# Performance work log

Measured on AMD Instinct MI355X. Metric: run time of the kernel, lower is better.

## Reference

```python
import jax, jax.numpy as jnp
import numpy as np

AC_KERNEL = 5


def deconv(x, w, stride):
    """torch ConvTranspose2d(k=3, p=1, bias=False), stride 1 or 2 (output_padding=1).
    w has torch layout [Cin, Cout, kH, kW]."""
    wk = jnp.transpose(w, (1, 0, 2, 3))[:, :, ::-1, ::-1]  # OIHW, spatially flipped
    dn = ('NCHW', 'OIHW', 'NCHW')
    if stride == 1:
        return jax.lax.conv_general_dilated(x, wk, (1, 1), ((1, 1), (1, 1)), dimension_numbers=dn)
    # stride 2: dilate input, pad (k-1-p, k-1-p+op) = (1, 2) -> doubles H, W
    return jax.lax.conv_general_dilated(x, wk, (1, 1), ((1, 2), (1, 2)),
                                        lhs_dilation=(2, 2), dimension_numbers=dn)


def sepconv(feat, kv, kh, K):
    """Per-pixel adaptive separable convolution (Niklaus SepConv).
    feat: [B,C,H,W]; kv, kh: [B,K,H,W]. Replication-pad by K//2, then
    out[b,c,y,x] = sum_{i,j} pad[b,c,y+i,x+j] * kv[b,i,y,x] * kh[b,j,y,x]."""
    pad = K // 2
    B, C, H, W = feat.shape
    p = jnp.pad(feat, ((0, 0), (0, 0), (pad, pad), (pad, pad)), mode='edge')
    out = jnp.zeros_like(feat)
    for i in range(K):  # small fixed loop over kernel taps
        row = p[:, :, i:i + H, :]  # [B,C,H,W+2*pad]
        horiz = row[:, :, :, 0:W] * kh[:, 0:1]
        for j in range(1, K):
            horiz = horiz + row[:, :, :, j:j + W] * kh[:, j:j + 1]
        out = out + kv[:, i:i + 1] * horiz
    return out


def fusion(feat, kv, kh, mask):
    tmp = sepconv(feat, kv, kh, AC_KERNEL)
    return mask * tmp + (1.0 - mask) * feat


def setup_inputs() -> dict:
    key = jax.random.key(0)
    ks = jax.random.split(key, 20)
    B, G = 128, 64
    d = {'cont_feat': jax.random.normal(ks[0], (B, G, 8, 8), jnp.float32)}
    sizes = [8, 16, 32, 64]
    for li, s in enumerate(sizes):
        d[f'kv{li}'] = jax.random.uniform(ks[1 + 3 * li], (B, AC_KERNEL, s, s), jnp.float32)
        d[f'kh{li}'] = jax.random.uniform(ks[2 + 3 * li], (B, AC_KERNEL, s, s), jnp.float32)
        d[f'm{li}'] = jax.random.uniform(ks[3 + 3 * li], (B, 1, s, s), jnp.float32)
    wshapes = [(G, G * 8, 3, 3), (G * 8, G * 4, 3, 3), (G * 4, G * 2, 3, 3),
               (G * 2, G * 2, 3, 3), (G * 2, G, 3, 3), (G, 3, 3, 3)]
    for wi, ws in enumerate(wshapes):
        d[f'w{wi + 1}'] = jax.random.normal(ks[13 + wi], ws, jnp.float32) * 0.05
    return d


def reference(cont_feat, kv0, kh0, m0, kv1, kh1, m1, kv2, kh2, m2, kv3, kh3, m3,
              w1, w2, w3, w4, w5, w6):
    # kernel_layer = 4, no_mask = False, use_bn = False
    feat_8 = fusion(cont_feat, kv0, kh0, m0)                      # [B,G,8,8]
    feat_16 = jax.nn.relu(deconv(feat_8, w1, 2))                  # [B,8G,16,16]
    feat_16 = fusion(feat_16, kv1, kh1, m1)
    h = jax.nn.relu(deconv(feat_16, w2, 1))                       # [B,4G,16,16]
    feat_32 = jax.nn.relu(deconv(h, w3, 2))                       # [B,2G,32,32]
    feat_32 = fusion(feat_32, kv2, kh2, m2)
    h = jax.nn.relu(deconv(feat_32, w4, 1))                       # [B,2G,32,32]
    h = jax.nn.relu(deconv(h, w5, 2))                             # [B,G,64,64]
    out = jnp.tanh(deconv(h, w6, 1))                              # [B,3,64,64]
    out = fusion(out, kv3, kh3, m3)
    return (out, feat_8, feat_16, feat_32)
```

## Files before the change

### kernel.cpp

```cpp
#include <hip/hip_runtime.h>
#include <math.h>

typedef short v8s __attribute__((ext_vector_type(8)));
typedef float v16f __attribute__((ext_vector_type(16)));

__device__ inline unsigned short f2bf(float f) {
    union { float f; unsigned u; } c; c.f = f;
    unsigned r = (c.u + 0x7fffu + ((c.u >> 16) & 1u)) >> 16;
    return (unsigned short)r;
}

template<int LW>
__global__ __launch_bounds__(256) void fusion2_kernel(
        const float* __restrict__ feat, const float* __restrict__ kv,
        const float* __restrict__ kh, const float* __restrict__ m,
        float* __restrict__ out, int C, int CH, int H, int lhw) {
    constexpr int W = 1 << LW;
    const int t = blockIdx.x * 256 + threadIdx.x;
    const int hw = H << LW;
    const int b = t >> lhw;
    const int pix = t & (hw - 1);
    const int x = pix & (W - 1);
    const int y = pix >> LW;
    const int lane = threadIdx.x & 63;
    const int rowbase = (lane & ~(W - 1)) << 2;

    const int c0 = blockIdx.y * CH;

    const float mv = m[(size_t)b * hw + pix];
    float kvv[5], khv[5];
#pragma unroll
    for (int i = 0; i < 5; i++) {
        kvv[i] = kv[((size_t)b * 5 + i) * hw + pix];
        khv[i] = kh[((size_t)b * 5 + i) * hw + pix];
    }
    int idx[5];
#pragma unroll
    for (int j = 0; j < 5; j++) {
        int xx = x + j - 2; xx = xx < 0 ? 0 : (xx >= W ? W - 1 : xx);
        idx[j] = rowbase + (xx << 2);
    }
    int roff[5];
#pragma unroll
    for (int i = 0; i < 5; i++) {
        int yy = y + i - 2; yy = yy < 0 ? 0 : (yy >= H ? H - 1 : yy);
        roff[i] = (yy << LW) + x;
    }

    const float* fbase = feat + ((size_t)b * C + c0) * hw;
    float* obase = out + ((size_t)b * C + c0) * hw + pix;
    const float om = 1.f - mv;

#pragma unroll 4
    for (int cc = 0; cc < CH; cc++) {
        const float* q = fbase + (size_t)cc * hw;
        float s = 0.f;
        float fv = 0.f;
#pragma unroll
        for (int i = 0; i < 5; i++) {
            float v = q[roff[i]];
            if (i == 2) fv = v;
            int vb = __float_as_int(v);
            float h = 0.f;
#pragma unroll
            for (int j = 0; j < 5; j++) {
                float nv = __int_as_float(
                    __builtin_amdgcn_ds_bpermute(idx[j], vb));
                h += nv * khv[j];
            }
            s += kvv[i] * h;
        }
        obase[(size_t)cc * hw] = mv * s + om * fv;
    }
}

__global__ __launch_bounds__(256) void nchw_to_nhwc_bf16(
        const float* __restrict__ in, unsigned short* __restrict__ out,
        int C, int H, int W, int lw, int lc2) {
    extern __shared__ unsigned short sm_t[];
    const int y = blockIdx.x, b = blockIdx.y;
    const int Cp = C + 8;
    const int tid = threadIdx.x;
    for (int i = tid; i < C * W; i += 256) {
        int x = i & (W - 1), c = i >> lw;
        float v = in[(((size_t)b * C + c) * H + y) * W + x];
        sm_t[x * Cp + c] = f2bf(v);
    }
    __syncthreads();
    const unsigned* s32 = (const unsigned*)sm_t;
    unsigned* o32 = (unsigned*)(out + (((size_t)b * H + y) * W) * C);
    const int n32 = (W * C) >> 1;
    for (int i = tid; i < n32; i += 256) {
        int x = i >> lc2;
        int c2 = i - (x << lc2);
        o32[i] = s32[x * (Cp >> 1) + c2];
    }
}

__global__ __launch_bounds__(256) void repack_w_frag(
        const float* __restrict__ w, unsigned short* __restrict__ wk,
        int Cin, int Cout, int flip) {
    int idx = blockIdx.x * 256 + threadIdx.x;
    if (idx >= Cin * Cout) return;
    int ci = idx / Cout, co = idx - ci * Cout;
    const float* src = w + (size_t)idx * 9;
    const int nCb = Cout >> 5, nH = Cin >> 4;
    const size_t inner = (size_t)((((ci >> 3) & 1) * 32 + (co & 31)) * 8 + (ci & 7));
#pragma unroll
    for (int k = 0; k < 9; k++) {
        int t = flip ? (8 - k) : k;
        size_t blk = ((size_t)t * nCb + (co >> 5)) * nH + (ci >> 4);
        wk[(blk << 9) + inner] = f2bf(src[k]);
    }
}

template<int W, int TH, int LW>
__global__ __launch_bounds__(256) void conv3x3_mfma(
        const unsigned short* __restrict__ X,
        const unsigned short* __restrict__ Wk,
        unsigned short* __restrict__ out, int Cin, int Cout, int H) {
    constexpr int TP = (TH + 2) * (W + 2);
    __shared__ unsigned short sB[TP * 40];
    const int tid = threadIdx.x;
    const int lane = tid & 63, wv = tid >> 6;
    const int wm = wv >> 1, wn = wv & 1;
    const int y0 = blockIdx.x * TH;
    const int coB = blockIdx.y * 128 + wm * 64;
    const int b = blockIdx.z;
    const int n = lane & 31, kg = lane >> 5;
    const int p0 = wn * 64 + n, p1 = p0 + 32;
    const int r0 = p0 >> LW, c0 = p0 & (W - 1);
    const int r1 = p1 >> LW, c1 = p1 & (W - 1);
    const int bo0 = (r0 * (W + 2) + c0) * 40 + kg * 8;
    const int bo1 = (r1 * (W + 2) + c1) * 40 + kg * 8;
    v16f acc00 = {}, acc01 = {}, acc10 = {}, acc11 = {};
    const size_t cbStride = (size_t)(Cin >> 4) << 9;
    const size_t tStride  = (size_t)(Cout >> 5) * cbStride;
    const unsigned short* Af = Wk + (size_t)(coB >> 5) * cbStride + (lane << 3);
    const unsigned short* Xb = X + (size_t)b * H * W * Cin;

    for (int ci0 = 0; ci0 < Cin; ci0 += 32) {
        for (int i = tid; i < TP * 4; i += 256) {
            int pix = i >> 2, part = i & 3;
            int py = pix / (W + 2), px = pix - py * (W + 2);
            int gy = y0 + py - 1, gx = px - 1;
            uint4 v = make_uint4(0u, 0u, 0u, 0u);
            if (gy >= 0 && gy < H && (unsigned)gx < (unsigned)W)
                v = *(const uint4*)(Xb + ((size_t)(gy * W + gx)) * Cin + ci0 + part * 8);
            *(uint4*)(sB + pix * 40 + part * 8) = v;
        }
        __syncthreads();
#pragma unroll
        for (int t = 0; t < 9; t++) {
            const int ky = t / 3, kx = t - ky * 3;
            const int toff = (ky * (W + 2) + kx) * 40;
#pragma unroll
            for (int kh = 0; kh < 2; kh++) {
                const unsigned short* ap =
                    Af + (size_t)t * tStride + (size_t)(((ci0 >> 4) + kh) << 9);
                v8s A0 = *(const v8s*)(ap);
                v8s A1 = *(const v8s*)(ap + cbStride);
                v8s B0 = *(const v8s*)(sB + bo0 + toff + kh * 16);
                v8s B1 = *(const v8s*)(sB + bo1 + toff + kh * 16);
                acc00 = __builtin_amdgcn_mfma_f32_32x32x16_bf16(A0, B0, acc00, 0, 0, 0);
                acc01 = __builtin_amdgcn_mfma_f32_32x32x16_bf16(A0, B1, acc01, 0, 0, 0);
                acc10 = __builtin_amdgcn_mfma_f32_32x32x16_bf16(A1, B0, acc10, 0, 0, 0);
                acc11 = __builtin_amdgcn_mfma_f32_32x32x16_bf16(A1, B1, acc11, 0, 0, 0);
            }
        }
        __syncthreads();
    }
    unsigned short* ob = out + (size_t)b * H * W * Cout;
#pragma unroll
    for (int sm = 0; sm < 2; sm++) {
        v16f a0 = sm ? acc10 : acc00;
        v16f a1 = sm ? acc11 : acc01;
        const int cobase = coB + sm * 32 + 4 * kg;
        unsigned short* q0p = ob + ((size_t)((y0 + r0) * W + c0)) * Cout + cobase;
        unsigned short* q1p = ob + ((size_t)((y0 + r1) * W + c1)) * Cout + cobase;
#pragma unroll
        for (int r2 = 0; r2 < 4; r2++) {
            ushort4 q0, q1; float v;
            v = a0[4 * r2 + 0]; v = v > 0.f ? v : 0.f; q0.x = f2bf(v);
            v = a0[4 * r2 + 1]; v = v > 0.f ? v : 0.f; q0.y = f2bf(v);
            v = a0[4 * r2 + 2]; v = v > 0.f ? v : 0.f; q0.z = f2bf(v);
            v = a0[4 * r2 + 3]; v = v > 0.f ? v : 0.f; q0.w = f2bf(v);
            *(ushort4*)(q0p + 8 * r2) = q0;
            v = a1[4 * r2 + 0]; v = v > 0.f ? v : 0.f; q1.x = f2bf(v);
            v = a1[4 * r2 + 1]; v = v > 0.f ? v : 0.f; q1.y = f2bf(v);
            v = a1[4 * r2 + 2]; v = v > 0.f ? v : 0.f; q1.z = f2bf(v);
            v = a1[4 * r2 + 3]; v = v > 0.f ? v : 0.f; q1.w = f2bf(v);
            *(ushort4*)(q1p + 8 * r2) = q1;
        }
    }
}

template<int W, int TH, int NWN, int NWM, int LW>
__global__ __launch_bounds__(256) void deconv2_mfma(
        const unsigned short* __restrict__ X,
        const unsigned short* __restrict__ Wk,
        float* __restrict__ out, int Cin, int Cout, int Hin) {
    constexpr int ROWS = NWN * TH + 1;
    constexpr int NPIX = ROWS * (W + 1);
    __shared__ unsigned short sB[NPIX * 40];
    const int tid = threadIdx.x;
    const int lane = tid & 63, wv = tid >> 6;
    const int wm = wv / NWN, wn = wv % NWN;
    const int n = lane & 31, kg = lane >> 5;
    const int y0 = blockIdx.x * (NWN * TH);
    const int coB = (blockIdx.y * NWM + wm) * 64;
    const int b = blockIdx.z;
    const int Yl = wn * TH + (n >> LW);
    const int Xl = n & (W - 1);
    v16f zero = {};
    v16f acc[2][2][2];
#pragma unroll
    for (int i = 0; i < 2; i++)
#pragma unroll
        for (int j = 0; j < 2; j++)
#pragma unroll
            for (int s = 0; s < 2; s++) acc[i][j][s] = zero;
    const unsigned short* Xb = X + (size_t)b * Hin * W * Cin;
    const size_t cbStride = (size_t)(Cin >> 4) << 9;
    const size_t tStride  = (size_t)(Cout >> 5) * cbStride;
    const unsigned short* Af = Wk + (size_t)(coB >> 5) * cbStride + (lane << 3);
    const int PY[3] = {1, 0, 1}, DY[3] = {1, 0, 0};

    for (int ci0 = 0; ci0 < Cin; ci0 += 32) {
        for (int i = tid; i < NPIX * 4; i += 256) {
            int pix = i >> 2, part = i & 3;
            int py_ = pix / (W + 1), px_ = pix - py_ * (W + 1);
            int gy = y0 + py_, gx = px_;
            uint4 v = make_uint4(0u, 0u, 0u, 0u);
            if (gy < Hin && gx < W)
                v = *(const uint4*)(Xb + ((size_t)(gy * W + gx)) * Cin + ci0 + part * 8);
            *(uint4*)(sB + pix * 40 + part * 8) = v;
        }
        __syncthreads();
#pragma unroll
        for (int ky = 0; ky < 3; ky++) {
#pragma unroll
            for (int kx = 0; kx < 3; kx++) {
                const int py = PY[ky], dy = DY[ky];
                const int px = PY[kx], dx = DY[kx];
                const int t = ky * 3 + kx;
                const int boff = ((Yl + dy) * (W + 1) + (Xl + dx)) * 40 + kg * 8;
#pragma unroll
                for (int kh = 0; kh < 2; kh++) {
                    const unsigned short* ap =
                        Af + (size_t)t * tStride + (size_t)(((ci0 >> 4) + kh) << 9);
                    v8s B  = *(const v8s*)(sB + boff + kh * 16);
                    v8s A0 = *(const v8s*)(ap);
                    v8s A1 = *(const v8s*)(ap + cbStride);
                    acc[py][px][0] = __builtin_amdgcn_mfma_f32_32x32x16_bf16(A0, B, acc[py][px][0], 0, 0, 0);
                    acc[py][px][1] = __builtin_amdgcn_mfma_f32_32x32x16_bf16(A1, B, acc[py][px][1], 0, 0, 0);
                }
            }
        }
        __syncthreads();
    }
    const int Wo = 2 * W, Ho = 2 * Hin;
    const int yin = y0 + Yl;
#pragma unroll
    for (int py = 0; py < 2; py++) {
        const int oy = 2 * yin + py;
#pragma unroll
        for (int sm = 0; sm < 2; sm++) {
            const int cobase = coB + sm * 32 + 4 * kg;
#pragma unroll
            for (int r = 0; r < 16; r++) {
                int co = cobase + (r & 3) + 8 * (r >> 2);
                float v0 = acc[py][0][sm][r]; v0 = v0 > 0.f ? v0 : 0.f;
                float v1 = acc[py][1][sm][r]; v1 = v1 > 0.f ? v1 : 0.f;
                *(float2*)(out + (((size_t)(b * Cout + co) * Ho + oy) * Wo + 2 * Xl)) =
                    make_float2(v0, v1);
            }
        }
    }
}

__global__ __launch_bounds__(256) void conv_s1_c3_tanh_kernel(
        const float* __restrict__ in, const float* __restrict__ w,
        float* __restrict__ out, int Cin, int H, int W) {
    __shared__ float sIn[8][18][19];
    __shared__ float sW[8][3][9];
    const int tid = threadIdx.x;
    const int r = tid >> 4, c = tid & 15;
    const int ntx = W >> 4;
    const int tx0 = (blockIdx.x % ntx) << 4, ty0 = (blockIdx.x / ntx) << 4;
    const int b = blockIdx.z;
    const int hw = H * W;
    float acc[3] = {0.f, 0.f, 0.f};
    for (int ci0 = 0; ci0 < Cin; ci0 += 8) {
        for (int i = tid; i < 8 * 18 * 18; i += 256) {
            int ci = i / 324, rr = i % 324, ly = rr / 18, lx = rr % 18;
            int gy = ty0 + ly - 1, gx = tx0 + lx - 1;
            float v = 0.f;
            if (gy >= 0 && gy < H && gx >= 0 && gx < W)
                v = in[(size_t)(b * Cin + ci0 + ci) * hw + gy * W + gx];
            sIn[ci][ly][lx] = v;
        }
        for (int i = tid; i < 8 * 3 * 9; i += 256) {
            int ci = i / 27, rr = i % 27, co = rr / 9, k = rr % 9;
            sW[ci][co][k] = w[(size_t)((ci0 + ci) * 3 + co) * 9 + (8 - k)];
        }
        __syncthreads();
#pragma unroll
        for (int ci = 0; ci < 8; ci++) {
            float v00 = sIn[ci][r][c],     v01 = sIn[ci][r][c + 1],     v02 = sIn[ci][r][c + 2];
            float v10 = sIn[ci][r + 1][c], v11 = sIn[ci][r + 1][c + 1], v12 = sIn[ci][r + 1][c + 2];
            float v20 = sIn[ci][r + 2][c], v21 = sIn[ci][r + 2][c + 1], v22 = sIn[ci][r + 2][c + 2];
#pragma unroll
            for (int co = 0; co < 3; co++) {
                const float* wp = &sW[ci][co][0];
                acc[co] += v00 * wp[0] + v01 * wp[1] + v02 * wp[2]
                         + v10 * wp[3] + v11 * wp[4] + v12 * wp[5]
                         + v20 * wp[6] + v21 * wp[7] + v22 * wp[8];
            }
        }
        __syncthreads();
    }
#pragma unroll
    for (int co = 0; co < 3; co++)
        out[(size_t)(b * 3 + co) * hw + (ty0 + r) * W + tx0 + c] = tanhf(acc[co]);
}

extern "C" void kernel_launch(void* const* d_in, const int* in_sizes, int n_in,
                              void* d_out, int out_size, void* d_ws, size_t ws_size,
                              hipStream_t stream) {
    const float* cont = (const float*)d_in[0];
    const float* kv0 = (const float*)d_in[1];
    const float* kh0 = (const float*)d_in[2];
    const float* m0  = (const float*)d_in[3];
    const float* kv1 = (const float*)d_in[4];
    const float* kh1 = (const float*)d_in[5];
    const float* m1  = (const float*)d_in[6];
    const float* kv2 = (const float*)d_in[7];
    const float* kh2 = (const float*)d_in[8];
    const float* m2  = (const float*)d_in[9];
    const float* kv3 = (const float*)d_in[10];
    const float* kh3 = (const float*)d_in[11];
    const float* m3  = (const float*)d_in[12];
    const float* w1  = (const float*)d_in[13];
    const float* w2  = (const float*)d_in[14];
    const float* w3  = (const float*)d_in[15];
    const float* w4  = (const float*)d_in[16];
    const float* w5  = (const float*)d_in[17];
    const float* w6  = (const float*)d_in[18];

    float* out = (float*)d_out;
    float* f8  = out + 1572864;
    float* f16 = out + 2097152;
    float* f32 = out + 18874368;

    char* ws = (char*)d_ws;

    float* A0 = (float*)ws;
    unsigned short* X8  = (unsigned short*)(ws + 67108864);
    unsigned short* Wk1 = (unsigned short*)(ws + 68157440);

    fusion2_kernel<3><<<dim3(32, 4), 256, 0, stream>>>(
        cont, kv0, kh0, m0, f8, 64, 16, 8, 6);
    nchw_to_nhwc_bf16<<<dim3(8, 128), 256, 8 * 72 * 2, stream>>>(f8, X8, 64, 8, 8, 3, 5);
    repack_w_frag<<<128, 256, 0, stream>>>(w1, Wk1, 64, 512, 0);
    deconv2_mfma<8, 4, 2, 2, 3><<<dim3(1, 4, 128), 256, 0, stream>>>(
        X8, Wk1, A0, 64, 512, 8);
    fusion2_kernel<4><<<dim3(128, 32), 256, 0, stream>>>(
        A0, kv1, kh1, m1, f16, 512, 16, 16, 8);

    unsigned short* X16 = (unsigned short*)ws;
    unsigned short* h1b = (unsigned short*)(ws + 67108864);
    unsigned short* Wk3 = (unsigned short*)(ws + 83886080);
    unsigned short* Wk2 = (unsigned short*)(ws + 84475904);
    nchw_to_nhwc_bf16<<<dim3(16, 128), 256, 16 * 520 * 2, stream>>>(
        f16, X16, 512, 16, 16, 4, 8);
    repack_w_frag<<<512, 256, 0, stream>>>(w2, Wk2, 512, 256, 1);
    conv3x3_mfma<16, 8, 4><<<dim3(2, 2, 128), 256, 0, stream>>>(
        X16, Wk2, h1b, 512, 256, 16);
    repack_w_frag<<<128, 256, 0, stream>>>(w3, Wk3, 256, 128, 0);
    float* t32 = (float*)ws;
    deconv2_mfma<16, 2, 2, 2, 4><<<dim3(4, 1, 128), 256, 0, stream>>>(
        h1b, Wk3, t32, 256, 128, 16);
    fusion2_kernel<5><<<dim3(512, 8), 256, 0, stream>>>(
        t32, kv2, kh2, m2, f32, 128, 16, 32, 10);

    unsigned short* Wk4  = (unsigned short*)ws;
    unsigned short* Wk5  = (unsigned short*)(ws + 294912);
    unsigned short* X32q = (unsigned short*)(ws + 524288);
    unsigned short* h2b  = (unsigned short*)(ws + 8912896);
    float* h3q = (float*)(ws + 17301504);
    float* tq  = (float*)(ws + 50855936);
    repack_w_frag<<<64, 256, 0, stream>>>(w4, Wk4, 128, 128, 1);
    repack_w_frag<<<32, 256, 0, stream>>>(w5, Wk5, 128, 64, 0);
    for (int q = 0; q < 4; q++) {
        size_t bo = (size_t)q * 32;
        const float* f32q = f32 + bo * 128 * 1024;
        nchw_to_nhwc_bf16<<<dim3(32, 32), 256, 32 * 136 * 2, stream>>>(
            f32q, X32q, 128, 32, 32, 5, 6);
        conv3x3_mfma<32, 4, 5><<<dim3(8, 1, 32), 256, 0, stream>>>(
            X32q, Wk4, h2b, 128, 128, 32);
        deconv2_mfma<32, 1, 4, 1, 5><<<dim3(8, 1, 32), 256, 0, stream>>>(
            h2b, Wk5, h3q, 128, 64, 32);
        conv_s1_c3_tanh_kernel<<<dim3(16, 1, 32), 256, 0, stream>>>(h3q, w6, tq, 64, 64, 64);
        fusion2_kernel<6><<<dim3(512, 1), 256, 0, stream>>>(
            tq, kv3 + bo * 5 * 4096, kh3 + bo * 5 * 4096, m3 + bo * 4096,
            out + bo * 3 * 4096, 3, 3, 64, 12);
    }
}
```

Measured before the change: 1.059 ms.

## Double-buffer LDS input tiles with register prefetch in conv and deconv kernels

Both MFMA convolution kernels now keep two LDS buffers. Each thread loads the next 32-channel input slice into registers before the current slice's MFMA work, then writes it to the alternate buffer afterwards. This lets global-load latency overlap compute and halves the barriers per channel step. In exchange it doubles LDS use and adds prefetch registers, which may lower occupancy.

```diff
diff --git a/kernel.cpp b/kernel.cpp
--- a/kernel.cpp
+++ b/kernel.cpp
@@ -120,7 +120,9 @@
         const unsigned short* __restrict__ Wk,
         unsigned short* __restrict__ out, int Cin, int Cout, int H) {
     constexpr int TP = (TH + 2) * (W + 2);
-    __shared__ unsigned short sB[TP * 40];
+    constexpr int NIT = TP * 4;
+    constexpr int NLD = (NIT + 255) / 256;
+    __shared__ unsigned short sB[2][TP * 40];
     const int tid = threadIdx.x;
     const int lane = tid & 63, wv = tid >> 6;
     const int wm = wv >> 1, wn = wv & 1;
@@ -139,17 +141,41 @@
     const unsigned short* Af = Wk + (size_t)(coB >> 5) * cbStride + (lane << 3);
     const unsigned short* Xb = X + (size_t)b * H * W * Cin;
 
-    for (int ci0 = 0; ci0 < Cin; ci0 += 32) {
-        for (int i = tid; i < TP * 4; i += 256) {
-            int pix = i >> 2, part = i & 3;
-            int py = pix / (W + 2), px = pix - py * (W + 2);
-            int gy = y0 + py - 1, gx = px - 1;
-            uint4 v = make_uint4(0u, 0u, 0u, 0u);
-            if (gy >= 0 && gy < H && (unsigned)gx < (unsigned)W)
-                v = *(const uint4*)(Xb + ((size_t)(gy * W + gx)) * Cin + ci0 + part * 8);
-            *(uint4*)(sB + pix * 40 + part * 8) = v;
-        }
-        __syncthreads();
+    const unsigned short* ldp[NLD];
+    int sto[NLD];
+#pragma unroll
+    for (int s = 0; s < NLD; s++) {
+        int i = tid + s * 256;
+        bool slot = (i < NIT);
+        int pix = i >> 2, part = i & 3;
+        int py = pix / (W + 2), px = pix - py * (W + 2);
+        int gy = y0 + py - 1, gx = px - 1;
+        bool ok = slot && gy >= 0 && gy < H && (unsigned)gx < (unsigned)W;
+        ldp[s] = ok ? Xb + ((size_t)(gy * W + gx)) * Cin + part * 8 : nullptr;
+        sto[s] = slot ? pix * 40 + part * 8 : -1;
+    }
+
+    uint4 pre[NLD];
+#pragma unroll
+    for (int s = 0; s < NLD; s++)
+        pre[s] = ldp[s] ? *(const uint4*)(ldp[s]) : make_uint4(0u, 0u, 0u, 0u);
+#pragma unroll
+    for (int s = 0; s < NLD; s++)
+        if (sto[s] >= 0) *(uint4*)(sB[0] + sto[s]) = pre[s];
+    __syncthreads();
+
+    const int NK = Cin >> 5;
+    for (int kk = 0; kk < NK; kk++) {
+        const int cur = kk & 1;
+        const int ci0 = kk << 5;
+        const bool more = (kk + 1 < NK);
+        if (more) {
+#pragma unroll
+            for (int s = 0; s < NLD; s++)
+                pre[s] = ldp[s] ? *(const uint4*)(ldp[s] + ci0 + 32)
+                                : make_uint4(0u, 0u, 0u, 0u);
+        }
+        const unsigned short* sC = sB[cur];
 #pragma unroll
         for (int t = 0; t < 9; t++) {
             const int ky = t / 3, kx = t - ky * 3;
@@ -160,15 +186,21 @@
                     Af + (size_t)t * tStride + (size_t)(((ci0 >> 4) + kh) << 9);
                 v8s A0 = *(const v8s*)(ap);
                 v8s A1 = *(const v8s*)(ap + cbStride);
-                v8s B0 = *(const v8s*)(sB + bo0 + toff + kh * 16);
-                v8s B1 = *(const v8s*)(sB + bo1 + toff + kh * 16);
+                v8s B0 = *(const v8s*)(sC + bo0 + toff + kh * 16);
+                v8s B1 = *(const v8s*)(sC + bo1 + toff + kh * 16);
                 acc00 = __builtin_amdgcn_mfma_f32_32x32x16_bf16(A0, B0, acc00, 0, 0, 0);
                 acc01 = __builtin_amdgcn_mfma_f32_32x32x16_bf16(A0, B1, acc01, 0, 0, 0);
                 acc10 = __builtin_amdgcn_mfma_f32_32x32x16_bf16(A1, B0, acc10, 0, 0, 0);
                 acc11 = __builtin_amdgcn_mfma_f32_32x32x16_bf16(A1, B1, acc11, 0, 0, 0);
             }
         }
-        __syncthreads();
+        if (more) {
+            unsigned short* sN = sB[cur ^ 1];
+#pragma unroll
+            for (int s = 0; s < NLD; s++)
+                if (sto[s] >= 0) *(uint4*)(sN + sto[s]) = pre[s];
+            __syncthreads();
+        }
     }
     unsigned short* ob = out + (size_t)b * H * W * Cout;
 #pragma unroll
@@ -202,7 +234,9 @@
         float* __restrict__ out, int Cin, int Cout, int Hin) {
     constexpr int ROWS = NWN * TH + 1;
     constexpr int NPIX = ROWS * (W + 1);
-    __shared__ unsigned short sB[NPIX * 40];
+    constexpr int NIT = NPIX * 4;
+    constexpr int NLD = (NIT + 255) / 256;
+    __shared__ unsigned short sB[2][NPIX * 40];
     const int tid = threadIdx.x;
     const int lane = tid & 63, wv = tid >> 6;
     const int wm = wv / NWN, wn = wv % NWN;
@@ -226,17 +260,41 @@
     const unsigned short* Af = Wk + (size_t)(coB >> 5) * cbStride + (lane << 3);
     const int PY[3] = {1, 0, 1}, DY[3] = {1, 0, 0};
 
-    for (int ci0 = 0; ci0 < Cin; ci0 += 32) {
-        for (int i = tid; i < NPIX * 4; i += 256) {
-            int pix = i >> 2, part = i & 3;
-            int py_ = pix / (W + 1), px_ = pix - py_ * (W + 1);
-            int gy = y0 + py_, gx = px_;
-            uint4 v = make_uint4(0u, 0u, 0u, 0u);
-            if (gy < Hin && gx < W)
-                v = *(const uint4*)(Xb + ((size_t)(gy * W + gx)) * Cin + ci0 + part * 8);
-            *(uint4*)(sB + pix * 40 + part * 8) = v;
-        }
-        __syncthreads();
+    const unsigned short* ldp[NLD];
+    int sto[NLD];
+#pragma unroll
+    for (int s = 0; s < NLD; s++) {
+        int i = tid + s * 256;
+        bool slot = (i < NIT);
+        int pix = i >> 2, part = i & 3;
+        int py_ = pix / (W + 1), px_ = pix - py_ * (W + 1);
+        int gy = y0 + py_, gx = px_;
+        bool ok = slot && gy < Hin && gx < W;
+        ldp[s] = ok ? Xb + ((size_t)(gy * W + gx)) * Cin + part * 8 : nullptr;
+        sto[s] = slot ? pix * 40 + part * 8 : -1;
+    }
+
+    uint4 pre[NLD];
+#pragma unroll
+    for (int s = 0; s < NLD; s++)
+        pre[s] = ldp[s] ? *(const uint4*)(ldp[s]) : make_uint4(0u, 0u, 0u, 0u);
+#pragma unroll
+    for (int s = 0; s < NLD; s++)
+        if (sto[s] >= 0) *(uint4*)(sB[0] + sto[s]) = pre[s];
+    __syncthreads();
+
+    const int NK = Cin >> 5;
+    for (int kk = 0; kk < NK; kk++) {
+        const int cur = kk & 1;
+        const int ci0 = kk << 5;
+        const bool more = (kk + 1 < NK);
+        if (more) {
+#pragma unroll
+            for (int s = 0; s < NLD; s++)
+                pre[s] = ldp[s] ? *(const uint4*)(ldp[s] + ci0 + 32)
+                                : make_uint4(0u, 0u, 0u, 0u);
+        }
+        const unsigned short* sC = sB[cur];
 #pragma unroll
         for (int ky = 0; ky < 3; ky++) {
 #pragma unroll
@@ -249,7 +307,7 @@
                 for (int kh = 0; kh < 2; kh++) {
                     const unsigned short* ap =
                         Af + (size_t)t * tStride + (size_t)(((ci0 >> 4) + kh) << 9);
-                    v8s B  = *(const v8s*)(sB + boff + kh * 16);
+                    v8s B  = *(const v8s*)(sC + boff + kh * 16);
                     v8s A0 = *(const v8s*)(ap);
                     v8s A1 = *(const v8s*)(ap + cbStride);
                     acc[py][px][0] = __builtin_amdgcn_mfma_f32_32x32x16_bf16(A0, B, acc[py][px][0], 0, 0, 0);
@@ -257,7 +315,13 @@
                 }
             }
         }
-        __syncthreads();
+        if (more) {
+            unsigned short* sN = sB[cur ^ 1];
+#pragma unroll
+            for (int s = 0; s < NLD; s++)
+                if (sto[s] >= 0) *(uint4*)(sN + sto[s]) = pre[s];
+            __syncthreads();
+        }
     }
     const int Wo = 2 * W, Ho = 2 * Hin;
     const int yin = y0 + Yl;
```

New measurement: 1.045 ms. Within noise of the previous version (-1.3%).
